# Performance work log

Hardware: AMD Instinct MI355X
Metric: run time of the kernel (lower is better)

Reference implementation:

```python
import jax, jax.numpy as jnp
import numpy as np

N_HEAD = 16


def setup_inputs() -> dict:
    key = jax.random.key(0)
    ks = jax.random.split(key, 5)
    B, T, C = 4, 2048, 1024
    # torch Linear stored as [out,in]; we use [in,out] so x @ W matches x @ W_t.T
    return {
        "x": jax.random.normal(ks[0], (B, T, C), jnp.float32),
        "c_attn_w": jax.random.normal(ks[1], (C, 3 * C), jnp.float32) * 0.02,
        "c_attn_b": jax.random.normal(ks[2], (3 * C,), jnp.float32) * 0.02,
        "c_proj_w": jax.random.normal(ks[3], (C, C), jnp.float32) * 0.02,
        "c_proj_b": jax.random.normal(ks[4], (C,), jnp.float32) * 0.02,
    }


def reference(x, c_attn_w, c_attn_b, c_proj_w, c_proj_b):
    B, T, C = x.shape
    H = N_HEAD
    d = C // H
    qkv = x @ c_attn_w + c_attn_b                      # [B,T,3C]
    q, k, v = jnp.split(qkv, 3, axis=2)
    q = q.reshape(B, T, H, d).transpose(0, 2, 1, 3)    # [B,H,T,d]
    k = k.reshape(B, T, H, d).transpose(0, 2, 1, 3)
    v = v.reshape(B, T, H, d).transpose(0, 2, 1, 3)
    scale = 1.0 / jnp.sqrt(jnp.asarray(d, x.dtype))
    w = jnp.einsum("bhqd,bhkd->bhqk", q, k) * scale    # [B,H,T,T]
    causal = jnp.tril(jnp.ones((T, T), bool))
    w = jnp.where(causal, w, jnp.asarray(-jnp.inf, w.dtype))
    w = jax.nn.softmax(w, axis=-1)
    y = jnp.einsum("bhqk,bhkd->bhqd", w, v)            # [B,H,T,d]
    y = y.transpose(0, 2, 1, 3).reshape(B, T, C)
    return y @ c_proj_w + c_proj_b
```

## Files before the change

kernel.cpp:

```cpp
#include <hip/hip_runtime.h>
#include <hip/hip_bf16.h>
#include <stdint.h>

#define DEV __device__ __forceinline__

typedef __attribute__((ext_vector_type(8))) short short8;
typedef __attribute__((ext_vector_type(8))) _Float16 half8;
typedef __attribute__((ext_vector_type(2))) __fp16 fp16x2;
typedef __attribute__((ext_vector_type(4))) float floatx4;
typedef __attribute__((ext_vector_type(16))) float floatx16;

DEV unsigned short f2bf(float f) {
  union { float f; uint32_t u; } v; v.f = f;
  uint32_t u = v.u;
  u += 0x7fffu + ((u >> 16) & 1u);
  return (unsigned short)(u >> 16);
}
DEV unsigned short f2h(float f) {
  union { _Float16 h; unsigned short u; } c; c.h = (_Float16)f; return c.u;
}
DEV void async_cp16(const unsigned short* g, unsigned short* l) {
  __builtin_amdgcn_global_load_lds(
      (const __attribute__((address_space(1))) uint32_t*)g,
      (__attribute__((address_space(3))) uint32_t*)l, 16, 0, 0);
}

__global__ __launch_bounds__(256)
void cvt_x_kernel(const float* __restrict__ x, unsigned short* __restrict__ xb) {
  const size_t i = ((size_t)blockIdx.x * 256 + threadIdx.x) * 4;
  const float4 f = *(const float4*)(x + i);
  ushort4 w;
  w.x = f2bf(f.x); w.y = f2bf(f.y); w.z = f2bf(f.z); w.w = f2bf(f.w);
  *(ushort4*)(xb + i) = w;
}

__global__ __launch_bounds__(256)
void transpose_w_kernel(const float* __restrict__ W, unsigned short* __restrict__ Wt,
                        int K, int N) {
  __shared__ float tile[64][65];
  const int k0 = blockIdx.y * 64, n0 = blockIdx.x * 64;
  const int tr = threadIdx.x >> 4;
  const int tc = (threadIdx.x & 15) * 4;
#pragma unroll
  for (int it = 0; it < 4; ++it) {
    const int k = tr + it * 16;
    const float4 f = *(const float4*)(W + (size_t)(k0 + k) * N + n0 + tc);
    tile[k][tc + 0] = f.x; tile[k][tc + 1] = f.y;
    tile[k][tc + 2] = f.z; tile[k][tc + 3] = f.w;
  }
  __syncthreads();
#pragma unroll
  for (int it = 0; it < 4; ++it) {
    const int n = tr + it * 16;
    ushort4 w;
    w.x = f2bf(tile[tc + 0][n]); w.y = f2bf(tile[tc + 1][n]);
    w.z = f2bf(tile[tc + 2][n]); w.w = f2bf(tile[tc + 3][n]);
    *(ushort4*)(Wt + (size_t)(n0 + n) * K + k0 + tc) = w;
  }
}

template <int EPI>
__global__ __launch_bounds__(256)
void gemm_bt_kernel(const unsigned short* __restrict__ A,
                    const unsigned short* __restrict__ Bt,
                    const float* __restrict__ bias, int M, int N, int K,
                    unsigned short* __restrict__ qws,
                    unsigned short* __restrict__ kws,
                    unsigned short* __restrict__ vws,
                    float* __restrict__ out) {
  __shared__ __align__(16) unsigned short As[128 * 32];
  __shared__ __align__(16) unsigned short Bs[128 * 32];
  const int tid = threadIdx.x;
  const int wid = tid >> 6, lane = tid & 63;
  const int quad = lane >> 4, l16 = lane & 15;
  const int wm = wid >> 1, wn = wid & 1;
  const int rowA0 = blockIdx.y * 128;
  const int colB0 = blockIdx.x * 128;

  const int srow = wid * 32 + (lane >> 2);
  const int sko = (lane & 3) * 8;
  const unsigned short* gA0 = A + (size_t)(rowA0 + srow) * K + sko;
  const unsigned short* gA1 = A + (size_t)(rowA0 + srow + 16) * K + sko;
  const unsigned short* gB0 = Bt + (size_t)(colB0 + srow) * K + sko;
  const unsigned short* gB1 = Bt + (size_t)(colB0 + srow + 16) * K + sko;
  unsigned short* lA0 = &As[(wid * 128 + 0) * 8];
  unsigned short* lA1 = &As[(wid * 128 + 64) * 8];
  unsigned short* lB0 = &Bs[(wid * 128 + 0) * 8];
  unsigned short* lB1 = &Bs[(wid * 128 + 64) * 8];

  floatx4 acc[4][4];
#pragma unroll
  for (int i = 0; i < 4; ++i)
#pragma unroll
    for (int j = 0; j < 4; ++j) acc[i][j] = (floatx4){0.f, 0.f, 0.f, 0.f};

  for (int kt = 0; kt < K; kt += 32) {
    __syncthreads();
    async_cp16(gA0 + kt, lA0);
    async_cp16(gA1 + kt, lA1);
    async_cp16(gB0 + kt, lB0);
    async_cp16(gB1 + kt, lB1);
    __syncthreads();

    short8 af[4], bfr[4];
#pragma unroll
    for (int i = 0; i < 4; ++i) {
      af[i] = *(const short8*)&As[(wm * 64 + i * 16 + l16) * 32 + quad * 8];
      bfr[i] = *(const short8*)&Bs[(wn * 64 + i * 16 + l16) * 32 + quad * 8];
    }
#pragma unroll
    for (int i = 0; i < 4; ++i)
#pragma unroll
      for (int j = 0; j < 4; ++j)
        acc[i][j] =
            __builtin_amdgcn_mfma_f32_16x16x32_bf16(af[i], bfr[j], acc[i][j], 0, 0, 0);
  }

#pragma unroll
  for (int i = 0; i < 4; ++i) {
#pragma unroll
    for (int j = 0; j < 4; ++j) {
      const int row0 = rowA0 + wm * 64 + i * 16 + quad * 4;
      const int col = colB0 + wn * 64 + j * 16 + l16;
      const float bv = bias[col];
#pragma unroll
      for (int r = 0; r < 4; ++r) {
        const float v = acc[i][j][r] + bv;
        const int R = row0 + r;
        if constexpr (EPI == 0) {
          const int b = R >> 11, t = R & 2047;
          const int which = col >> 10, c = col & 1023;
          const int h = c >> 6, dd = c & 63;
          const size_t bh = (size_t)(b * 16 + h);
          if (which == 0)
            qws[(bh * 2048 + t) * 64 + dd] = f2bf(v * 0.125f);
          else if (which == 1)
            kws[(bh * 2048 + t) * 64 + dd] = f2bf(v);
          else
            vws[(bh * 64 + dd) * 2048 + t] = f2h(v);
        } else {
          out[(size_t)R * N + col] = v;
        }
      }
    }
  }
}

__global__ __launch_bounds__(256, 2)
void attn_mfma_kernel(const unsigned short* __restrict__ qws,
                      const unsigned short* __restrict__ kws,
                      const unsigned short* __restrict__ vws,
                      unsigned short* __restrict__ yws) {
  constexpr int T = 2048, D = 64;
  __shared__ __align__(16) unsigned short Ks[128 * 72];
  __shared__ __align__(16) unsigned short Vs[64 * 136];
  const int tid = threadIdx.x;
  const int wid = tid >> 6, lane = tid & 63;
  const int hf = lane >> 5, l32 = lane & 31;
  const int bh = blockIdx.x;
  const int qt = 15 - (int)blockIdx.y;
  const int qbase = qt * 128;
  const unsigned short* Qp = qws + (size_t)bh * T * D;
  const unsigned short* Kp = kws + (size_t)bh * T * D;
  const unsigned short* Vp = vws + (size_t)bh * D * T;

  const int q = qbase + wid * 32 + l32;
  short8 qf[4];
#pragma unroll
  for (int s = 0; s < 4; ++s)
    qf[s] = *(const short8*)(Qp + (size_t)q * D + s * 16 + hf * 8);

  floatx16 Oacc[2];
#pragma unroll
  for (int mt2 = 0; mt2 < 2; ++mt2)
#pragma unroll
    for (int i = 0; i < 16; ++i) Oacc[mt2][i] = 0.f;
  float mrun = -1e30f, lrun = 0.f;

  for (int kt = 0; kt <= qt; ++kt) {
    const int kb = kt * 128;
    __syncthreads();
#pragma unroll
    for (int it = 0; it < 4; ++it) {
      const int e = it * 256 + tid;
      {
        const int row = e >> 3, c = (e & 7) * 8;
        *(short8*)&Ks[row * 72 + c] =
            *(const short8*)(Kp + (size_t)(kb + row) * D + c);
      }
      {
        const int row = e >> 4, c = (e & 15) * 8;
        *(short8*)&Vs[row * 136 + c] =
            *(const short8*)(Vp + (size_t)row * T + kb + c);
      }
    }
    __syncthreads();

    const bool diag = (kt == qt);
    const int mtmax = diag ? (wid + 1) : 4;

    floatx16 S[4];
#pragma unroll
    for (int mt = 0; mt < 4; ++mt)
      if (mt < mtmax)
#pragma unroll
        for (int i = 0; i < 16; ++i) S[mt][i] = 0.f;

#pragma unroll
    for (int s = 0; s < 4; ++s) {
#pragma unroll
      for (int mt = 0; mt < 4; ++mt)
        if (mt < mtmax) {
          const short8 kf =
              *(const short8*)&Ks[(mt * 32 + l32) * 72 + s * 16 + hf * 8];
          S[mt] = __builtin_amdgcn_mfma_f32_32x32x16_bf16(kf, qf[s], S[mt], 0, 0, 0);
        }
    }

    if (diag) {
#pragma unroll
      for (int mt = 0; mt < 4; ++mt)
        if (mt == wid) {
#pragma unroll
          for (int r = 0; r < 16; ++r) {
            const int intra = (r & 3) + 8 * (r >> 2) + 4 * hf;
            if (intra > l32) S[mt][r] = -1e30f;
          }
        }
    }

    float tmax = -1e30f;
#pragma unroll
    for (int mt = 0; mt < 4; ++mt)
      if (mt < mtmax)
#pragma unroll
        for (int r = 0; r < 16; ++r) tmax = fmaxf(tmax, S[mt][r]);
    tmax = fmaxf(tmax, __shfl_xor(tmax, 32, 64));
    const float mn = fmaxf(mrun, tmax);
    const float alpha = __expf(mrun - mn);
    mrun = mn;

    float tsum = 0.f;
    uint32_t pk[4][8];
#pragma unroll
    for (int mt = 0; mt < 4; ++mt)
      if (mt < mtmax)
#pragma unroll
        for (int t = 0; t < 8; ++t) {
          const float pa = __expf(S[mt][2 * t] - mn);
          const float pb = __expf(S[mt][2 * t + 1] - mn);
          tsum += pa + pb;
          union { fp16x2 h; uint32_t u; } cv;
          cv.h = __builtin_amdgcn_cvt_pkrtz(pa, pb);
          pk[mt][t] = cv.u;
        }
    tsum += __shfl_xor(tsum, 32, 64);
    lrun = lrun * alpha + tsum;
#pragma unroll
    for (int mt2 = 0; mt2 < 2; ++mt2)
#pragma unroll
      for (int i = 0; i < 16; ++i) Oacc[mt2][i] *= alpha;

    const int smax = 2 * mtmax;
#pragma unroll
    for (int s = 0; s < 8; ++s)
      if (s < smax) {
        const int mt = s >> 1;
        const int bo = 4 * (s & 1);
        const uint32_t own0 = hf ? pk[mt][bo + 2] : pk[mt][bo];
        const uint32_t own1 = hf ? pk[mt][bo + 3] : pk[mt][bo + 1];
        const uint32_t sendA = hf ? pk[mt][bo] : pk[mt][bo + 2];
        const uint32_t sendB = hf ? pk[mt][bo + 1] : pk[mt][bo + 3];
        const uint32_t recvA = (uint32_t)__shfl_xor((int)sendA, 32, 64);
        const uint32_t recvB = (uint32_t)__shfl_xor((int)sendB, 32, 64);
        union { uint32_t u[4]; half8 h; } bb;
        bb.u[0] = hf ? recvA : own0;
        bb.u[1] = hf ? recvB : own1;
        bb.u[2] = hf ? own0 : recvA;
        bb.u[3] = hf ? own1 : recvB;
#pragma unroll
        for (int mt2 = 0; mt2 < 2; ++mt2) {
          const half8 vf =
              *(const half8*)&Vs[(mt2 * 32 + l32) * 136 + s * 16 + hf * 8];
          Oacc[mt2] = __builtin_amdgcn_mfma_f32_32x32x16_f16(vf, bb.h, Oacc[mt2], 0, 0, 0);
        }
      }
  }

  const float invl = 1.0f / lrun;
  const int b_ = bh >> 4, h_ = bh & 15;
  unsigned short* yrow = yws + ((size_t)(b_ * 2048 + q)) * 1024 + h_ * 64;
#pragma unroll
  for (int mt2 = 0; mt2 < 2; ++mt2)
#pragma unroll
    for (int t = 0; t < 8; ++t) {
      const int d0 = mt2 * 32 + 2 * (t & 1) + 8 * (t >> 1) + 4 * hf;
      const uint32_t ua = f2bf(Oacc[mt2][2 * t] * invl);
      const uint32_t ub = f2bf(Oacc[mt2][2 * t + 1] * invl);
      *(uint32_t*)&yrow[d0] = ua | (ub << 16);
    }
}

extern "C" void kernel_launch(void* const* d_in, const int* in_sizes, int n_in,
                              void* d_out, int out_size, void* d_ws, size_t ws_size,
                              hipStream_t stream) {
  (void)in_sizes; (void)n_in; (void)out_size;
  const float* x = (const float*)d_in[0];
  const float* attn_w = (const float*)d_in[1];
  const float* attn_b = (const float*)d_in[2];
  const float* proj_w = (const float*)d_in[3];
  const float* proj_b = (const float*)d_in[4];
  float* out = (float*)d_out;

  const size_t NQ = 8388608;
  unsigned short* qws = (unsigned short*)d_ws;
  unsigned short* kws = qws + NQ;
  unsigned short* vws = kws + NQ;
  unsigned short* yws = vws + NQ;
  unsigned short* xb  = yws + NQ;
  unsigned short* wta = xb + NQ;
  unsigned short* wtp = wta + 3072 * 1024;
  if (ws_size < (5 * NQ + 4 * 1024 * 1024) * sizeof(unsigned short)) return;

  cvt_x_kernel<<<dim3(8192), dim3(256), 0, stream>>>(x, xb);
  transpose_w_kernel<<<dim3(48, 16), dim3(256), 0, stream>>>(attn_w, wta, 1024, 3072);
  transpose_w_kernel<<<dim3(16, 16), dim3(256), 0, stream>>>(proj_w, wtp, 1024, 1024);

  gemm_bt_kernel<0><<<dim3(24, 64), dim3(256), 0, stream>>>(
      xb, wta, attn_b, 8192, 3072, 1024, qws, kws, vws, nullptr);
  attn_mfma_kernel<<<dim3(64, 16), dim3(256), 0, stream>>>(qws, kws, vws, yws);
  gemm_bt_kernel<1><<<dim3(8, 64), dim3(256), 0, stream>>>(
      yws, wtp, proj_b, 8192, 1024, 1024, nullptr, nullptr, nullptr, out);
}
```

Before: 280.0 us.

## Replace GEMM with 256x256-tile double-buffered pipelined kernel with XOR-swizzled LDS

Replaces the 128x128 single-buffered bf16 GEMM with a 256x256 tile, 512-thread kernel. It double-buffers LDS with asynchronous global-to-LDS loads interleaved across four compute phases per K-tile, using explicit waitcnt and barrier control plus setprio around the MFMA bursts. It also XOR-swizzles the LDS layout to avoid bank conflicts and remaps block IDs for L2 locality. The aim is to hide load latency and raise data reuse in both projection GEMMs. In exchange the loop is hardcoded to K=1024 (16 tiles of 64), uses 128KB of LDS and many accumulator registers, and the larger tiles leave few workgroups per GPU (128 for the output projection).

```diff
diff --git a/kernel.cpp b/kernel.cpp
--- a/kernel.cpp
+++ b/kernel.cpp
@@ -59,73 +59,127 @@
   }
 }
 
+#define BAR asm volatile("s_barrier" ::: "memory")
+#define LGK0 asm volatile("s_waitcnt lgkmcnt(0)" ::: "memory")
+#define VMW(N) asm volatile("s_waitcnt vmcnt(" #N ")" ::: "memory")
+#define NOW (void)0
+#define NOSTG (void)0
+
 template <int EPI>
-__global__ __launch_bounds__(256)
-void gemm_bt_kernel(const unsigned short* __restrict__ A,
+__global__ __launch_bounds__(512, 2)
+void gemm256_kernel(const unsigned short* __restrict__ A,
                     const unsigned short* __restrict__ Bt,
                     const float* __restrict__ bias, int M, int N, int K,
+                    int nbx,
                     unsigned short* __restrict__ qws,
                     unsigned short* __restrict__ kws,
                     unsigned short* __restrict__ vws,
                     float* __restrict__ out) {
-  __shared__ __align__(16) unsigned short As[128 * 32];
-  __shared__ __align__(16) unsigned short Bs[128 * 32];
+  (void)M;
+  __shared__ __align__(16) unsigned short L[2][32768];
   const int tid = threadIdx.x;
   const int wid = tid >> 6, lane = tid & 63;
   const int quad = lane >> 4, l16 = lane & 15;
-  const int wm = wid >> 1, wn = wid & 1;
-  const int rowA0 = blockIdx.y * 128;
-  const int colB0 = blockIdx.x * 128;
-
-  const int srow = wid * 32 + (lane >> 2);
-  const int sko = (lane & 3) * 8;
-  const unsigned short* gA0 = A + (size_t)(rowA0 + srow) * K + sko;
-  const unsigned short* gA1 = A + (size_t)(rowA0 + srow + 16) * K + sko;
-  const unsigned short* gB0 = Bt + (size_t)(colB0 + srow) * K + sko;
-  const unsigned short* gB1 = Bt + (size_t)(colB0 + srow + 16) * K + sko;
-  unsigned short* lA0 = &As[(wid * 128 + 0) * 8];
-  unsigned short* lA1 = &As[(wid * 128 + 64) * 8];
-  unsigned short* lB0 = &Bs[(wid * 128 + 0) * 8];
-  unsigned short* lB1 = &Bs[(wid * 128 + 64) * 8];
-
-  floatx4 acc[4][4];
-#pragma unroll
-  for (int i = 0; i < 4; ++i)
+  const int wm = wid >> 2, wn = wid & 3;
+
+  const int nwg = (int)gridDim.x;
+  const int bid = (int)blockIdx.x;
+  const int swz = (bid & 7) * (nwg >> 3) + (bid >> 3);
+  const int bx = swz % nbx, by = swz / nbx;
+  const int rowA0 = by * 256, colB0 = bx * 256;
+
+  const int srow = tid >> 3;
+  const int ksrc = (((tid & 7) ^ (srow & 7)) << 3);
+  const unsigned short* pA00 = A + (size_t)(rowA0 + 0   + srow) * K + ksrc;
+  const unsigned short* pA01 = A + (size_t)(rowA0 + 64  + srow) * K + ksrc;
+  const unsigned short* pA10 = A + (size_t)(rowA0 + 128 + srow) * K + ksrc;
+  const unsigned short* pA11 = A + (size_t)(rowA0 + 192 + srow) * K + ksrc;
+  const unsigned short* pB00 = Bt + (size_t)(colB0 + 0   + srow) * K + ksrc;
+  const unsigned short* pB01 = Bt + (size_t)(colB0 + 64  + srow) * K + ksrc;
+  const unsigned short* pB10 = Bt + (size_t)(colB0 + 128 + srow) * K + ksrc;
+  const unsigned short* pB11 = Bt + (size_t)(colB0 + 192 + srow) * K + ksrc;
+
+#define STG_A0(P, T) do { async_cp16(pA00 + (T)*64, &L[P][0     + wid*512]); \
+                          async_cp16(pA01 + (T)*64, &L[P][4096  + wid*512]); } while (0)
+#define STG_A1(P, T) do { async_cp16(pA10 + (T)*64, &L[P][8192  + wid*512]); \
+                          async_cp16(pA11 + (T)*64, &L[P][12288 + wid*512]); } while (0)
+#define STG_B0(P, T) do { async_cp16(pB00 + (T)*64, &L[P][16384 + wid*512]); \
+                          async_cp16(pB01 + (T)*64, &L[P][20480 + wid*512]); } while (0)
+#define STG_B1(P, T) do { async_cp16(pB10 + (T)*64, &L[P][24576 + wid*512]); \
+                          async_cp16(pB11 + (T)*64, &L[P][28672 + wid*512]); } while (0)
+#define STG_B01(P, T) do { STG_B0(P, T); STG_B1(P, T); } while (0)
+
+  floatx4 acc[8][4];
+#pragma unroll
+  for (int i = 0; i < 8; ++i)
 #pragma unroll
     for (int j = 0; j < 4; ++j) acc[i][j] = (floatx4){0.f, 0.f, 0.f, 0.f};
-
-  for (int kt = 0; kt < K; kt += 32) {
-    __syncthreads();
-    async_cp16(gA0 + kt, lA0);
-    async_cp16(gA1 + kt, lA1);
-    async_cp16(gB0 + kt, lB0);
-    async_cp16(gB1 + kt, lB1);
-    __syncthreads();
-
-    short8 af[4], bfr[4];
-#pragma unroll
-    for (int i = 0; i < 4; ++i) {
-      af[i] = *(const short8*)&As[(wm * 64 + i * 16 + l16) * 32 + quad * 8];
-      bfr[i] = *(const short8*)&Bs[(wn * 64 + i * 16 + l16) * 32 + quad * 8];
-    }
-#pragma unroll
-    for (int i = 0; i < 4; ++i)
-#pragma unroll
-      for (int j = 0; j < 4; ++j)
-        acc[i][j] =
-            __builtin_amdgcn_mfma_f32_16x16x32_bf16(af[i], bfr[j], acc[i][j], 0, 0, 0);
-  }
-
-#pragma unroll
-  for (int i = 0; i < 4; ++i) {
-#pragma unroll
-    for (int j = 0; j < 4; ++j) {
-      const int row0 = rowA0 + wm * 64 + i * 16 + quad * 4;
-      const int col = colB0 + wn * 64 + j * 16 + l16;
+  short8 bfrag[4];
+
+  STG_A0(0, 0); STG_A1(0, 0); STG_B0(0, 0); STG_B1(0, 0);
+  STG_B01(1, 1);
+  VMW(4);
+  BAR;
+
+#define PHASE(PAR, QM, KS, RB, STG, W)                                        \
+  {                                                                           \
+    short8 a_[4];                                                             \
+    _Pragma("unroll") for (int m_ = 0; m_ < 4; ++m_) {                        \
+      const int row_ = wm * 128 + ((QM)*4 + m_) * 16 + l16;                   \
+      a_[m_] = *(const short8*)&L[PAR][row_ * 64 +                            \
+                 ((((KS)*32) + quad * 8) ^ ((row_ & 7) << 3))];               \
+    }                                                                         \
+    if (RB) {                                                                 \
+      _Pragma("unroll") for (int n_ = 0; n_ < 4; ++n_) {                      \
+        const int row_ = wn * 64 + n_ * 16 + l16;                             \
+        bfrag[n_] = *(const short8*)&L[PAR][16384 + row_ * 64 +               \
+                 ((((KS)*32) + quad * 8) ^ ((row_ & 7) << 3))];               \
+      }                                                                       \
+    }                                                                         \
+    STG;                                                                      \
+    BAR;                                                                      \
+    LGK0;                                                                     \
+    __builtin_amdgcn_s_setprio(1);                                            \
+    _Pragma("unroll") for (int m_ = 0; m_ < 4; ++m_)                          \
+      _Pragma("unroll") for (int n_ = 0; n_ < 4; ++n_)                        \
+        acc[(QM)*4 + m_][n_] = __builtin_amdgcn_mfma_f32_16x16x32_bf16(       \
+            a_[m_], bfrag[n_], acc[(QM)*4 + m_][n_], 0, 0, 0);                \
+    __builtin_amdgcn_s_setprio(0);                                            \
+    W;                                                                        \
+    BAR;                                                                      \
+  }
+
+#define KTILE(PAR, S1, S2, S4, W4) \
+  PHASE(PAR, 0, 0, 1, S1, NOW)     \
+  PHASE(PAR, 1, 0, 0, S2, NOW)     \
+  PHASE(PAR, 0, 1, 1, NOSTG, NOW)  \
+  PHASE(PAR, 1, 1, 0, S4, W4)
+
+  for (int t0 = 0; t0 < 14; t0 += 2) {
+    KTILE(0, STG_A0(1, t0 + 1), STG_A1(1, t0 + 1), STG_B01(0, t0 + 2), VMW(4))
+    KTILE(1, STG_A0(0, t0 + 2), STG_A1(0, t0 + 2), STG_B01(1, t0 + 3), VMW(4))
+  }
+  KTILE(0, STG_A0(1, 15), STG_A1(1, 15), NOSTG, VMW(0))
+  KTILE(1, NOSTG, NOSTG, NOSTG, NOW)
+
+#undef KTILE
+#undef PHASE
+#undef STG_A0
+#undef STG_A1
+#undef STG_B0
+#undef STG_B1
+#undef STG_B01
+
+#pragma unroll
+  for (int mi = 0; mi < 8; ++mi) {
+#pragma unroll
+    for (int ni = 0; ni < 4; ++ni) {
+      const int row0 = rowA0 + wm * 128 + mi * 16 + quad * 4;
+      const int col = colB0 + wn * 64 + ni * 16 + l16;
       const float bv = bias[col];
 #pragma unroll
       for (int r = 0; r < 4; ++r) {
-        const float v = acc[i][j][r] + bv;
+        const float v = acc[mi][ni][r] + bv;
         const int R = row0 + r;
         if constexpr (EPI == 0) {
           const int b = R >> 11, t = R & 2047;
@@ -326,9 +380,9 @@
   transpose_w_kernel<<<dim3(48, 16), dim3(256), 0, stream>>>(attn_w, wta, 1024, 3072);
   transpose_w_kernel<<<dim3(16, 16), dim3(256), 0, stream>>>(proj_w, wtp, 1024, 1024);
 
-  gemm_bt_kernel<0><<<dim3(24, 64), dim3(256), 0, stream>>>(
-      xb, wta, attn_b, 8192, 3072, 1024, qws, kws, vws, nullptr);
+  gemm256_kernel<0><<<dim3(384), dim3(512), 0, stream>>>(
+      xb, wta, attn_b, 8192, 3072, 1024, 12, qws, kws, vws, nullptr);
   attn_mfma_kernel<<<dim3(64, 16), dim3(256), 0, stream>>>(qws, kws, vws, yws);
-  gemm_bt_kernel<1><<<dim3(8, 64), dim3(256), 0, stream>>>(
-      yws, wtp, proj_b, 8192, 1024, 1024, nullptr, nullptr, nullptr, out);
-}
+  gemm256_kernel<1><<<dim3(128), dim3(512), 0, stream>>>(
+      yws, wtp, proj_b, 8192, 1024, 1024, 4, nullptr, nullptr, nullptr, out);
+}
```

Result: no change. 283.3 us (+1.2%).
